# Optimization experiments

Measured on AMD Instinct MI355X. Metric: run time of the kernel, lower is better.

Reference implementation:

```python
import jax, jax.numpy as jnp
import numpy as np

L = 1.0
N = 1024
DT = 1e-7
NUM_STEPS = 128
P = 16  # param_x = param_y
DX = L / (N - 1)


def bilinear_resize(a, n):
    """Bilinear upsample a (P,P) map to (n,n), align_corners=True (matches F.interpolate)."""
    p = a.shape[0]
    coords = jnp.linspace(0.0, p - 1.0, n)
    i0 = jnp.floor(coords).astype(jnp.int32)
    i1 = jnp.minimum(i0 + 1, p - 1)
    w = (coords - i0).astype(a.dtype)
    rows = a[i0] * (1.0 - w)[:, None] + a[i1] * w[:, None]          # (n, p)
    return rows[:, i0] * (1.0 - w)[None, :] + rows[:, i1] * w[None, :]  # (n, n)


def setup_inputs() -> dict:
    key = jax.random.key(0)
    k1, k2, k3 = jax.random.split(key, 3)
    u0 = jax.random.normal(k1, (N, N), dtype=jnp.float32)
    alpha = jax.random.uniform(k2, (P, P), dtype=jnp.float32)
    kappa = jax.random.uniform(k3, (P, P), dtype=jnp.float32)
    return {"u0": u0, "alpha": alpha, "kappa": kappa}


def _simulate(u0, alpha, kappa):
    amap = bilinear_resize(alpha, N)[1:-1, 1:-1]  # interior diffusion coeff
    kmap = bilinear_resize(kappa, N)[1:-1, 1:-1]  # interior advection coeff
    dx2 = DX * DX

    def step(T, _):
        Tc = T[1:-1, 1:-1]
        T_xx = (T[:-2, 1:-1] - 2.0 * Tc + T[2:, 1:-1]) / dx2
        T_yy = (T[1:-1, :-2] - 2.0 * Tc + T[1:-1, 2:]) / dx2
        T_x = (T[2:, 1:-1] - T[:-2, 1:-1]) / (2.0 * DX)
        T_y = (T[1:-1, 2:] - T[1:-1, :-2]) / (2.0 * DX)
        interior = Tc - DT * kmap * (Tc * T_x + Tc * T_y) + DT * amap * (T_xx + T_yy)
        Tn = T.at[1:-1, 1:-1].set(interior)
        # Neumann-like boundary copies, same order as the torch code
        Tn = Tn.at[0, :].set(Tn[1, :])
        Tn = Tn.at[-1, :].set(Tn[-2, :])
        Tn = Tn.at[:, 0].set(Tn[:, 1])
        Tn = Tn.at[:, -1].set(Tn[:, -2])
        return Tn, T  # record the state BEFORE the step (as torch does)

    _, ys = jax.lax.scan(step, u0, None, length=NUM_STEPS)
    return ys[1:]  # (NUM_STEPS-1, N, N)


def reference(u0, alpha, kappa):
    return _simulate(u0, alpha, kappa)
```

## Files before the change

### kernel.cpp

```cpp
#include <hip/hip_runtime.h>

#define GN   1024
#define GNN  (GN * GN)
#define GP   16
#define NOUT 127
#define TILE 64
#define KST  16
#define SZ   96
#define LSTR 100
#define NRB  24
#define NCB  24
#define NTHR 576


__device__ __forceinline__ void coord16(int t, int& c0, int& c1, float& w) {
    double c = (double)t * (15.0 / 1023.0);
    c0 = (int)c;
    c1 = c0 + 1 > 15 ? 15 : c0 + 1;
    w  = (float)(c - (double)c0);
}

__device__ __forceinline__ float bilin16(const float* __restrict__ m,
                                         int i0, int i1, float wi,
                                         int j0, int j1, float wj) {
    float m00 = m[i0 * GP + j0];
    float m10 = m[i1 * GP + j0];
    float m01 = m[i0 * GP + j1];
    float m11 = m[i1 * GP + j1];
    float r0 = m00 * (1.0f - wi) + m10 * wi;
    float r1 = m01 * (1.0f - wi) + m11 * wi;
    return r0 * (1.0f - wj) + r1 * wj;
}

__device__ __forceinline__ float cellv(float C, float L, float R, float U, float D,
                                       float a2, float k2) {
    float s   = (D - U) + (R - L);
    float lap = fmaf(-4.0f, C, (U + D) + (L + R));
    return fmaf(a2, lap, fmaf(-k2, C * s, C));
}

__device__ __forceinline__ float4 rowcell(float4 v, float4 U, float4 D,
                                          float sl, float sr,
                                          float4 a2, float4 k2,
                                          bool isl, bool isr) {
    float L0 = isl ? v.x : sl;
    float C0 = isl ? v.y : v.x;
    float R0 = isl ? v.z : v.y;
    float U0 = isl ? U.y : U.x;
    float D0 = isl ? D.y : D.x;
    float L3 = isr ? v.y : v.z;
    float C3 = isr ? v.z : v.w;
    float R3 = isr ? v.w : sr;
    float U3 = isr ? U.z : U.w;
    float D3 = isr ? D.z : D.w;
    float4 nv;
    nv.x = cellv(C0,  L0,  R0,  U0,  D0,  a2.x, k2.x);
    nv.y = cellv(v.y, v.x, v.z, U.y, D.y, a2.y, k2.y);
    nv.z = cellv(v.z, v.y, v.w, U.z, D.z, a2.z, k2.z);
    nv.w = cellv(C3,  L3,  R3,  U3,  D3,  a2.w, k2.w);
    return nv;
}

__device__ __forceinline__ void lds_barrier() {
    __builtin_amdgcn_sched_barrier(0);
    asm volatile("s_waitcnt lgkmcnt(0)" ::: "memory");
    __builtin_amdgcn_s_barrier();
    __builtin_amdgcn_sched_barrier(0);
}

__global__ __launch_bounds__(256)
void resize_maps_kernel(const float* __restrict__ alpha,
                        const float* __restrict__ kappa,
                        float* __restrict__ a2map,
                        float* __restrict__ k2map) {
    int idx = blockIdx.x * 256 + threadIdx.x;
    if (idx >= GNN) return;
    int i = idx >> 10;
    int j = idx & (GN - 1);
    int ci = i < 1 ? 1 : (i > GN - 2 ? GN - 2 : i);
    int cj = j < 1 ? 1 : (j > GN - 2 ? GN - 2 : j);
    int i0, i1, j0, j1; float wi, wj;
    coord16(ci, i0, i1, wi);
    coord16(cj, j0, j1, wj);
    a2map[idx] = bilin16(alpha, i0, i1, wi, j0, j1, wj) * 0.1046529f;
    k2map[idx] = bilin16(kappa, i0, i1, wi, j0, j1, wj) * 5.115e-5f;
}

template <bool USE_WS>
__global__ __launch_bounds__(NTHR)
void fused_steps_kernel(const float* __restrict__ srcp,
                        const float* __restrict__ Aarg,
                        const float* __restrict__ Karg,
                        float* __restrict__ out,
                        int base)
{
    __shared__ float buf[2][SZ * LSTR];

    const int tid = threadIdx.x;
    const int rb  = tid / NCB;
    const int cb  = tid - rb * NCB;
    const int r0  = rb * 4;
    const int c4  = cb * 4;

    const int gi0 = blockIdx.y * TILE;
    const int gj0 = blockIdx.x * TILE;
    int oi = gi0 - KST; oi = oi < 0 ? 0 : (oi > GN - SZ ? GN - SZ : oi);
    int oj = gj0 - KST; oj = oj < 0 ? 0 : (oj > GN - SZ ? GN - SZ : oj);
    const int di = gi0 - oi;
    const int dj = gj0 - oj;

    const bool istop = (rb == 0), isbot = (rb == NRB - 1);
    const bool isl   = (cb == 0), isr   = (cb == NCB - 1);
    const bool core  = (rb >= (di >> 2)) && (rb < (di >> 2) + 16)
                    && (cb >= (dj >> 2)) && (cb < (dj >> 2) + 16);
    const int  tmax  = NOUT - base;

    const long gbase = (long)(oi + r0) * GN + oj + c4;

    const int ob  = r0 * LSTR + c4;
    const int ub  = (istop ? 0 : (r0 - 1)) * LSTR + c4;
    const int db  = (isbot ? (SZ - 1) : (r0 + 4)) * LSTR + c4;
    const int slo = r0 * LSTR + (isl ? 0 : (c4 - 1));
    const int sro = r0 * LSTR + (isr ? (SZ - 1) : (c4 + 4));

    float4 a2[4], k2[4];
    if (USE_WS) {
        #pragma unroll
        for (int q = 0; q < 4; ++q) {
            a2[q] = *(const float4*)(Aarg + gbase + q * GN);
            k2[q] = *(const float4*)(Karg + gbase + q * GN);
        }
    } else {
        #pragma unroll
        for (int q = 0; q < 4; ++q) {
            int gi = oi + r0 + q;
            int ci = gi < 1 ? 1 : (gi > GN - 2 ? GN - 2 : gi);
            int i0, i1; float wi;
            coord16(ci, i0, i1, wi);
            float av[4], kv[4];
            #pragma unroll
            for (int u = 0; u < 4; ++u) {
                int gj = oj + c4 + u;
                int cj = gj < 1 ? 1 : (gj > GN - 2 ? GN - 2 : gj);
                int j0, j1; float wj;
                coord16(cj, j0, j1, wj);
                av[u] = bilin16(Aarg, i0, i1, wi, j0, j1, wj) * 0.1046529f;
                kv[u] = bilin16(Karg, i0, i1, wi, j0, j1, wj) * 5.115e-5f;
            }
            a2[q] = make_float4(av[0], av[1], av[2], av[3]);
            k2[q] = make_float4(kv[0], kv[1], kv[2], kv[3]);
        }
    }

    float4 V[4];
    {
        float4 ld0 = *(const float4*)(srcp + gbase);
        float4 ld1 = *(const float4*)(srcp + gbase + GN);
        float4 ld2 = *(const float4*)(srcp + gbase + 2 * GN);
        float4 ld3 = *(const float4*)(srcp + gbase + 3 * GN);
        *(float4*)&buf[0][ob]            = ld0;
        *(float4*)&buf[0][ob + LSTR]     = ld1;
        *(float4*)&buf[0][ob + 2 * LSTR] = ld2;
        *(float4*)&buf[0][ob + 3 * LSTR] = ld3;
        V[0] = istop ? ld1 : ld0;
        V[1] = ld1;
        V[2] = ld2;
        V[3] = isbot ? ld2 : ld3;
    }
    __syncthreads();

    auto step = [&](const float* __restrict__ cur, float* __restrict__ nxt, int t) {
        float4 U = *(const float4*)(cur + ub);
        float4 D = *(const float4*)(cur + db);
        float sl0 = cur[slo];            float sr0 = cur[sro];
        float sl1 = cur[slo + LSTR];     float sr1 = cur[sro + LSTR];
        float sl2 = cur[slo + 2 * LSTR]; float sr2 = cur[sro + 2 * LSTR];
        float sl3 = cur[slo + 3 * LSTR]; float sr3 = cur[sro + 3 * LSTR];

        float4 Uop1 = istop ? U : V[0];
        float4 Dop2 = isbot ? D : V[3];

        float4 NV0 = rowcell(V[0], U,    V[1], sl0, sr0, a2[0], k2[0], isl, isr);
        float4 NV1 = rowcell(V[1], Uop1, V[2], sl1, sr1, a2[1], k2[1], isl, isr);
        float4 NV2 = rowcell(V[2], V[1], Dop2, sl2, sr2, a2[2], k2[2], isl, isr);
        float4 NV3 = rowcell(V[3], V[2], D,    sl3, sr3, a2[3], k2[3], isl, isr);
        if (istop) NV0 = NV1;
        if (isbot) NV3 = NV2;

        *(float4*)(nxt + ob)            = NV0;
        *(float4*)(nxt + ob + LSTR)     = NV1;
        *(float4*)(nxt + ob + 2 * LSTR) = NV2;
        *(float4*)(nxt + ob + 3 * LSTR) = NV3;

        if (core && t <= tmax) {
            float* slab = out + (long)(base + t - 1) * GNN;
            *(float4*)(slab + gbase)          = NV0;
            *(float4*)(slab + gbase + GN)     = NV1;
            *(float4*)(slab + gbase + 2 * GN) = NV2;
            *(float4*)(slab + gbase + 3 * GN) = NV3;
        }
        V[0] = NV0; V[1] = NV1; V[2] = NV2; V[3] = NV3;
        lds_barrier();
    };

    float* B0 = &buf[0][0];
    float* B1 = &buf[1][0];
    #pragma unroll 1
    for (int it = 0; it < KST / 2; ++it) {
        step(B0, B1, 2 * it + 1);
        step(B1, B0, 2 * it + 2);
    }
}

extern "C" void kernel_launch(void* const* d_in, const int* in_sizes, int n_in,
                              void* d_out, int out_size, void* d_ws, size_t ws_size,
                              hipStream_t stream) {
    const float* u0    = (const float*)d_in[0];
    const float* alpha = (const float*)d_in[1];
    const float* kappa = (const float*)d_in[2];
    float* out = (float*)d_out;

    dim3 grd(GN / TILE, GN / TILE, 1);

    bool use_ws = ws_size >= (size_t)2 * GNN * sizeof(float);

    if (use_ws) {
        float* a2map = (float*)d_ws;
        float* k2map = a2map + GNN;
        resize_maps_kernel<<<(GNN + 255) / 256, 256, 0, stream>>>(alpha, kappa, a2map, k2map);
        for (int b = 0; b < NOUT; b += KST) {
            const float* src = (b == 0) ? u0 : out + (long)(b - 1) * GNN;
            fused_steps_kernel<true><<<grd, NTHR, 0, stream>>>(src, a2map, k2map, out, b);
        }
    } else {
        for (int b = 0; b < NOUT; b += KST) {
            const float* src = (b == 0) ? u0 : out + (long)(b - 1) * GNN;
            fused_steps_kernel<false><<<grd, NTHR, 0, stream>>>(src, alpha, kappa, out, b);
        }
    }
}
```

Before: 210.5 us.

## Store only halo edges in LDS with transposed side columns for vector reads

Instead of keeping the full 96x96 tile in LDS, each thread writes only its top and bottom rows plus transposed left/right edge columns into separate planes. Neighbors then read four float4 loads (up, down, left-side column, right-side column) rather than two float4 and eight scalar loads. This cuts LDS read instructions and scalar bank traffic per step, at the cost of extra register shuffles to pack the column vectors and a more intricate indexing scheme.

```diff
diff --git a/kernel.cpp b/kernel.cpp
--- a/kernel.cpp
+++ b/kernel.cpp
@@ -7,10 +7,13 @@
 #define TILE 64
 #define KST  16
 #define SZ   96
-#define LSTR 100
 #define NRB  24
 #define NCB  24
 #define NTHR 576
+#define RST  100
+#define AXB  (NRB * 2 * RST)
+#define AXS  ((NCB + 1) * RST)
+#define PLN  (AXB + 2 * AXS)
 
 
 __device__ __forceinline__ void coord16(int t, int& c0, int& c1, float& w) {
@@ -94,7 +97,7 @@
                         float* __restrict__ out,
                         int base)
 {
-    __shared__ float buf[2][SZ * LSTR];
+    __shared__ float lds[2][PLN];
 
     const int tid = threadIdx.x;
     const int rb  = tid / NCB;
@@ -117,11 +120,14 @@
 
     const long gbase = (long)(oi + r0) * GN + oj + c4;
 
-    const int ob  = r0 * LSTR + c4;
-    const int ub  = (istop ? 0 : (r0 - 1)) * LSTR + c4;
-    const int db  = (isbot ? (SZ - 1) : (r0 + 4)) * LSTR + c4;
-    const int slo = r0 * LSTR + (isl ? 0 : (c4 - 1));
-    const int sro = r0 * LSTR + (isr ? (SZ - 1) : (c4 + 4));
+    const int uoff   = (istop ? 0 : (rb * 2 - 1)) * RST + c4;
+    const int doff   = (isbot ? (NRB * 2 - 1) : (rb * 2 + 2)) * RST + c4;
+    const int w0off  = (rb * 2) * RST + c4;
+    const int w3off  = (rb * 2 + 1) * RST + c4;
+    const int sloff  = AXB + cb * RST + rb * 4;
+    const int wsloff = AXB + (cb + 1) * RST + rb * 4;
+    const int sroff  = AXB + AXS + (cb + 1) * RST + rb * 4;
+    const int wsroff = AXB + AXS + cb * RST + rb * 4;
 
     float4 a2[4], k2[4];
     if (USE_WS) {
@@ -158,10 +164,10 @@
         float4 ld1 = *(const float4*)(srcp + gbase + GN);
         float4 ld2 = *(const float4*)(srcp + gbase + 2 * GN);
         float4 ld3 = *(const float4*)(srcp + gbase + 3 * GN);
-        *(float4*)&buf[0][ob]            = ld0;
-        *(float4*)&buf[0][ob + LSTR]     = ld1;
-        *(float4*)&buf[0][ob + 2 * LSTR] = ld2;
-        *(float4*)&buf[0][ob + 3 * LSTR] = ld3;
+        *(float4*)&lds[0][w0off]  = ld0;
+        *(float4*)&lds[0][w3off]  = ld3;
+        *(float4*)&lds[0][wsloff] = make_float4(ld0.w, ld1.w, ld2.w, ld3.w);
+        *(float4*)&lds[0][wsroff] = make_float4(ld0.x, ld1.x, ld2.x, ld3.x);
         V[0] = istop ? ld1 : ld0;
         V[1] = ld1;
         V[2] = ld2;
@@ -170,27 +176,25 @@
     __syncthreads();
 
     auto step = [&](const float* __restrict__ cur, float* __restrict__ nxt, int t) {
-        float4 U = *(const float4*)(cur + ub);
-        float4 D = *(const float4*)(cur + db);
-        float sl0 = cur[slo];            float sr0 = cur[sro];
-        float sl1 = cur[slo + LSTR];     float sr1 = cur[sro + LSTR];
-        float sl2 = cur[slo + 2 * LSTR]; float sr2 = cur[sro + 2 * LSTR];
-        float sl3 = cur[slo + 3 * LSTR]; float sr3 = cur[sro + 3 * LSTR];
+        float4 U  = *(const float4*)(cur + uoff);
+        float4 D  = *(const float4*)(cur + doff);
+        float4 SL = *(const float4*)(cur + sloff);
+        float4 SR = *(const float4*)(cur + sroff);
 
         float4 Uop1 = istop ? U : V[0];
         float4 Dop2 = isbot ? D : V[3];
 
-        float4 NV0 = rowcell(V[0], U,    V[1], sl0, sr0, a2[0], k2[0], isl, isr);
-        float4 NV1 = rowcell(V[1], Uop1, V[2], sl1, sr1, a2[1], k2[1], isl, isr);
-        float4 NV2 = rowcell(V[2], V[1], Dop2, sl2, sr2, a2[2], k2[2], isl, isr);
-        float4 NV3 = rowcell(V[3], V[2], D,    sl3, sr3, a2[3], k2[3], isl, isr);
+        float4 NV0 = rowcell(V[0], U,    V[1], SL.x, SR.x, a2[0], k2[0], isl, isr);
+        float4 NV1 = rowcell(V[1], Uop1, V[2], SL.y, SR.y, a2[1], k2[1], isl, isr);
+        float4 NV2 = rowcell(V[2], V[1], Dop2, SL.z, SR.z, a2[2], k2[2], isl, isr);
+        float4 NV3 = rowcell(V[3], V[2], D,    SL.w, SR.w, a2[3], k2[3], isl, isr);
         if (istop) NV0 = NV1;
         if (isbot) NV3 = NV2;
 
-        *(float4*)(nxt + ob)            = NV0;
-        *(float4*)(nxt + ob + LSTR)     = NV1;
-        *(float4*)(nxt + ob + 2 * LSTR) = NV2;
-        *(float4*)(nxt + ob + 3 * LSTR) = NV3;
+        *(float4*)(nxt + w0off)  = NV0;
+        *(float4*)(nxt + w3off)  = NV3;
+        *(float4*)(nxt + wsloff) = make_float4(NV0.w, NV1.w, NV2.w, NV3.w);
+        *(float4*)(nxt + wsroff) = make_float4(NV0.x, NV1.x, NV2.x, NV3.x);
 
         if (core && t <= tmax) {
             float* slab = out + (long)(base + t - 1) * GNN;
@@ -203,12 +207,10 @@
         lds_barrier();
     };
 
-    float* B0 = &buf[0][0];
-    float* B1 = &buf[1][0];
     #pragma unroll 1
     for (int it = 0; it < KST / 2; ++it) {
-        step(B0, B1, 2 * it + 1);
-        step(B1, B0, 2 * it + 2);
+        step(&lds[0][0], &lds[1][0], 2 * it + 1);
+        step(&lds[1][0], &lds[0][0], 2 * it + 2);
     }
 }
 
```

Result: no change. 212.5 us (+0.9%).
